# Performance work log

Hardware: AMD Instinct MI355X
Metric: run time of the kernel (lower is better)

## Reference

```python
import jax, jax.numpy as jnp
import numpy as np

B, L, D = 2, 1024, 1024
N = 64                 # ssm_state_dim
R = (D + 15) // 16     # dt_rank = ceil(dim/16) = 64
EPS = 1e-6


def setup_inputs() -> dict:
    key = jax.random.key(0)
    ks = jax.random.split(key, 12)
    s = 0.02
    return {
        "x": jax.random.normal(ks[0], (B, L, D), dtype=jnp.float32),
        "norm_w": jnp.ones((D,), jnp.float32),
        "Wx": jax.random.normal(ks[1], (R + 2 * N, D), jnp.float32) * s,
        "dtW": jax.random.normal(ks[2], (D, R), jnp.float32) * s,
        "dtb": jax.random.normal(ks[3], (D,), jnp.float32) * s,
        "A_log": jnp.zeros((D, N), jnp.float32),
        "Dskip": jnp.ones((D,), jnp.float32),
        "Wout": jax.random.normal(ks[4], (D, D), jnp.float32) * s,
        "selW": jax.random.normal(ks[5], (D, D), jnp.float32) * s,
        "selb": jax.random.normal(ks[6], (D,), jnp.float32) * s,
        "sel_gate": jnp.ones((D,), jnp.float32),
        "impW": jax.random.normal(ks[7], (N, D), jnp.float32) * s,
        "impb": jax.random.normal(ks[8], (N,), jnp.float32) * s,
        "gateW": jax.random.normal(ks[9], (D, D), jnp.float32) * s,
        "gateb": jax.random.normal(ks[10], (D,), jnp.float32) * s,
    }


def _rmsnorm(x, w):
    return x * jax.lax.rsqrt(jnp.mean(x * x, axis=-1, keepdims=True) + EPS) * w


def reference(x, norm_w, Wx, dtW, dtb, A_log, Dskip, Wout, selW, selb,
              sel_gate, impW, impb, gateW, gateb):
    xn = _rmsnorm(x, norm_w)                       # [B,L,D]
    xp = jnp.einsum('bld,kd->blk', xn, Wx)         # [B,L,R+2N]
    delta_r = xp[..., :R]
    B_ssm = xp[..., R:R + N]
    C_ssm = xp[..., R + N:]

    # selective masking
    sel = jax.nn.sigmoid((jnp.einsum('bld,kd->blk', xn, selW) + selb) * sel_gate)
    xn = xn * sel
    imp = jax.nn.sigmoid(jnp.einsum('bld,nd->bln', xn, impW) + impb)  # [B,L,N]

    delta = jax.nn.softplus(jnp.einsum('blr,dr->bld', delta_r, dtW) + dtb)  # [B,L,D]
    A = -jnp.exp(A_log)                            # [D,N]

    # gated update
    gate = jax.nn.sigmoid(jnp.einsum('bld,kd->blk', xn, gateW) + gateb)
    xn = xn * gate

    B_ssm = B_ssm * imp
    C_ssm = C_ssm * imp

    def step(h, inp):
        dt, bt, ct, xt = inp                       # [B,D],[B,N],[B,N],[B,D]
        dA = jnp.exp(dt[:, :, None] * A)           # [B,D,N]
        h = dA * h + dt[:, :, None] * bt[:, None, :] * xt[:, :, None]
        y = jnp.einsum('bdn,bn->bd', h, ct)
        return h, y

    h0 = jnp.zeros((B, D, N), x.dtype)
    xs = (jnp.moveaxis(delta, 1, 0), jnp.moveaxis(B_ssm, 1, 0),
          jnp.moveaxis(C_ssm, 1, 0), jnp.moveaxis(xn, 1, 0))
    _, ys = jax.lax.scan(step, h0, xs)             # ys: [L,B,D]
    y = jnp.moveaxis(ys, 0, 1)                     # [B,L,D]

    return jnp.einsum('bld,kd->blk', y + x * Dskip, Wout)
```

## Files before the change

### kernel.cpp

```cpp
#include <hip/hip_runtime.h>

typedef __attribute__((ext_vector_type(8))) short short8;
typedef __attribute__((ext_vector_type(4))) float f32x4;
typedef unsigned short u16;

__device__ __forceinline__ u16 f2bf(float f){
  unsigned int u = __float_as_uint(f);
  u += 0x7FFFu + ((u>>16)&1u);
  return (u16)(u>>16);
}
__device__ __forceinline__ float bf2f(u16 h){
  return __uint_as_float(((unsigned int)h)<<16);
}
__device__ __forceinline__ float sigm(float x){ return 1.f/(1.f+__expf(-x)); }

__device__ __forceinline__ float fexp2(float x){
#if __has_builtin(__builtin_amdgcn_exp2f)
  return __builtin_amdgcn_exp2f(x);
#else
  float r; asm("v_exp_f32 %0, %1" : "=v"(r) : "v"(x)); return r;
#endif
}

__device__ __forceinline__ void gl_lds(const u16* g, u16* l){
  __builtin_amdgcn_global_load_lds(
      (const __attribute__((address_space(1))) void*)g,
      (__attribute__((address_space(3))) void*)l, 16, 0, 0);
}

#define MDIM 2048
#define DDIM 1024
#define KDIM 1024
#define LOG2E 1.44269504f
#define NCHUNK 32
#define TCH 32
#define CVT_TOTAL 3473408

__global__ __launch_bounds__(256) void pre_k(
    const float* __restrict__ x, const float* __restrict__ nw,
    const float* __restrict__ selW, const float* __restrict__ Wx,
    const float* __restrict__ gateW, const float* __restrict__ impW,
    const float* __restrict__ Wout, const float* __restrict__ dtW,
    u16* __restrict__ xn,
    u16* __restrict__ dA, u16* __restrict__ dB, u16* __restrict__ dC,
    u16* __restrict__ dD)
{
  const int bx = blockIdx.x, tid = threadIdx.x;
  if (bx < 2048){
    float4 xv = ((const float4*)(x + (size_t)bx*DDIM))[tid];
    float s = xv.x*xv.x + xv.y*xv.y + xv.z*xv.z + xv.w*xv.w;
    #pragma unroll
    for (int m=1; m<64; m<<=1) s += __shfl_xor(s, m);
    __shared__ float red[4];
    if ((tid&63)==0) red[tid>>6] = s;
    __syncthreads();
    float tot = red[0]+red[1]+red[2]+red[3];
    float rs = rsqrtf(tot*(1.f/1024.f) + 1e-6f);
    float4 wv = ((const float4*)nw)[tid];
    ushort4 o;
    o.x=f2bf(xv.x*rs*wv.x); o.y=f2bf(xv.y*rs*wv.y);
    o.z=f2bf(xv.z*rs*wv.z); o.w=f2bf(xv.w*rs*wv.w);
    ((ushort4*)(xn + (size_t)bx*DDIM))[tid] = o;
  } else {
    int e = ((bx-2048)*256 + tid)*4;
    if (e >= CVT_TOTAL) return;
    const float4* s; u16* d;
    if (e < 1048576){ s=(const float4*)(selW+e); d=dA+e; }
    else if (e < 1245184){ int o=e-1048576; s=(const float4*)(Wx+o); d=dA+1048576+o; }
    else if (e < 2293760){ int o=e-1245184; s=(const float4*)(gateW+o); d=dB+o; }
    else if (e < 2359296){ int o=e-2293760; s=(const float4*)(impW+o); d=dB+1048576+o; }
    else if (e < 3407872){ int o=e-2359296; s=(const float4*)(Wout+o); d=dC+o; }
    else { int o=e-3407872; s=(const float4*)(dtW+o); d=dD+o; }
    float4 v = *s;
    ushort4 ov; ov.x=f2bf(v.x); ov.y=f2bf(v.y); ov.z=f2bf(v.z); ov.w=f2bf(v.w);
    *(ushort4*)d = ov;
  }
}

template<int MODE>
__device__ __forceinline__ void gemm_body(
    u16* smem,
    const u16* __restrict__ X, const u16* __restrict__ W,
    const float* __restrict__ b1, const float* __restrict__ b2,
    const float* __restrict__ b3, const u16* __restrict__ aux,
    u16* __restrict__ oBF, u16* __restrict__ oBF2,
    float* __restrict__ oF1, float* __restrict__ oF2, float* __restrict__ oF3)
{
  u16* const AsP[2] = { smem, smem + 4096 };
  u16* const BsP[2] = { smem + 8192, smem + 12288 };
  const int tid = threadIdx.x;
  const int wid = tid>>6, lane = tid&63;
  const int wr = wid>>1, wc = wid&1;
  const int lr = lane&15, lg = lane>>4;

  const int nx = gridDim.x;
  const int nwg = nx*gridDim.y;
  const int lin = blockIdx.y*nx + blockIdx.x;
  const int lt = (lin&7)*(nwg>>3) + (lin>>3);
  const int bm = (lt/nx)*64, bn = (lt%nx)*64;

  f32x4 acc[2][2];
  #pragma unroll
  for (int a0=0;a0<2;++a0)
    #pragma unroll
    for (int b0=0;b0<2;++b0) acc[a0][b0] = (f32x4){0.f,0.f,0.f,0.f};

  const int srow = wid*8 + (lane>>3);
  const int kslot = 8*((lane&7) ^ (lane>>3));
  const u16* ag = X + (size_t)(bm + srow)*KDIM + kslot;
  const u16* bg = W + (size_t)(bn + srow)*KDIM + kslot;
  const int lofs = wid*512;

  auto stage = [&](int buf, int kt){
    gl_lds(ag + kt, AsP[buf] + lofs);
    gl_lds(ag + (size_t)32*KDIM + kt, AsP[buf] + 2048 + lofs);
    gl_lds(bg + kt, BsP[buf] + lofs);
    gl_lds(bg + (size_t)32*KDIM + kt, BsP[buf] + 2048 + lofs);
  };

  stage(0, 0);
  stage(1, 64);
  asm volatile("s_waitcnt vmcnt(4)" ::: "memory");
  __builtin_amdgcn_s_barrier();

  int cur = 0;
  #pragma unroll
  for (int kt=0; kt<KDIM; kt+=64){
    short8 af[2][2], bfr[2][2];
    #pragma unroll
    for (int a0=0;a0<2;++a0){
      const int R = wr*32 + a0*16 + lr;
      #pragma unroll
      for (int kh=0;kh<2;++kh)
        af[a0][kh] = *(const short8*)(AsP[cur] + R*64 + ((kh*32 + lg*8) ^ ((lr&7)<<3)));
    }
    #pragma unroll
    for (int b0=0;b0<2;++b0){
      const int R = wc*32 + b0*16 + lr;
      #pragma unroll
      for (int kh=0;kh<2;++kh)
        bfr[b0][kh] = *(const short8*)(BsP[cur] + R*64 + ((kh*32 + lg*8) ^ ((lr&7)<<3)));
    }
    asm volatile("s_waitcnt lgkmcnt(0)" ::: "memory");
    __builtin_amdgcn_sched_barrier(0);
    __builtin_amdgcn_s_barrier();
    if (kt < KDIM-128)
      stage(cur, kt+128);
    #pragma unroll
    for (int kh=0;kh<2;++kh)
      #pragma unroll
      for (int a0=0;a0<2;++a0)
        #pragma unroll
        for (int b0=0;b0<2;++b0)
          acc[a0][b0] = __builtin_amdgcn_mfma_f32_16x16x32_bf16(af[a0][kh], bfr[b0][kh], acc[a0][b0], 0, 0, 0);
    __builtin_amdgcn_sched_barrier(0);
    if (kt < KDIM-128){
      asm volatile("s_waitcnt vmcnt(4)" ::: "memory");
      __builtin_amdgcn_s_barrier();
    } else if (kt < KDIM-64){
      asm volatile("s_waitcnt vmcnt(0)" ::: "memory");
      __builtin_amdgcn_s_barrier();
    }
    cur ^= 1;
  }

  const int colb = bn + wc*32;
  #pragma unroll
  for (int a0=0;a0<2;++a0){
    const int m0 = bm + wr*32 + a0*16 + lg*4;
    #pragma unroll
    for (int b0=0;b0<2;++b0){
      const int n = colb + b0*16 + lr;
      #pragma unroll
      for (int i=0;i<4;++i){
        const int m = m0 + i;
        float v = acc[a0][b0][i];
        if constexpr (MODE==0){
          if (n < 1024){
            float s = sigm((v + b1[n])*b2[n]);
            float xnv = bf2f(aux[(size_t)m*1024 + n]);
            oBF[(size_t)m*1024 + n] = f2bf(xnv*s);
          } else if (n < 1088){
            oBF2[(size_t)m*64 + (n-1024)] = f2bf(v);
          } else {
            oF2[(size_t)m*128 + (n-1088)] = v;
          }
        } else if constexpr (MODE==1){
          if (n < 1024){
            float g = sigm(v + b1[n]);
            oBF[(size_t)m*1024 + n] = f2bf(bf2f(aux[(size_t)m*1024 + n])*g);
          } else {
            int c = n-1024;
            float it = sigm(v + b2[c]);
            float bb = b3[(size_t)m*128 + c];
            float cc = b3[(size_t)m*128 + 64 + c];
            oF2[(size_t)m*64 + c] = bb*it;
            oF3[(size_t)m*64 + c] = cc*it;
          }
        } else {
          oF1[(size_t)m*1024 + n] = v;
        }
      }
    }
  }
}

template<int MODE>
__global__ __launch_bounds__(256) void gemm_bt(
    const u16* __restrict__ X, const u16* __restrict__ W,
    const float* __restrict__ b1, const float* __restrict__ b2,
    const float* __restrict__ b3, const u16* __restrict__ aux,
    u16* __restrict__ oBF, u16* __restrict__ oBF2,
    float* __restrict__ oF1, float* __restrict__ oF2, float* __restrict__ oF3)
{
  __shared__ __align__(16) u16 pool[16384];
  gemm_body<MODE>(pool, X, W, b1, b2, b3, aux, oBF, oBF2, oF1, oF2, oF3);
}

__global__ __launch_bounds__(256) void gemm1d_k(
    const u16* __restrict__ xn2, const u16* __restrict__ wsB,
    const float* __restrict__ gateb, const float* __restrict__ impb,
    const float* __restrict__ BCb,
    u16* __restrict__ xn316, float* __restrict__ BIp, float* __restrict__ CIp,
    const u16* __restrict__ dr, const u16* __restrict__ dtWb,
    const float* __restrict__ dtb, u16* __restrict__ delta16)
{
  __shared__ __align__(16) u16 pool[16384];
  if (blockIdx.z == 0){
    gemm_body<1>(pool, xn2, wsB, gateb, impb, BCb, xn2,
                 xn316, nullptr, nullptr, BIp, CIp);
    return;
  }
  if (blockIdx.x >= 16) return;
  u16* As = pool;
  u16* Bs = pool + 4096;
  const int tid = threadIdx.x;
  const int wid = tid>>6, lane = tid&63;
  const int wr = wid>>1, wc = wid&1;
  const int lr = lane&15, lg = lane>>4;
  const int bm = blockIdx.y*64, bn = blockIdx.x*64;

  const int srow = wid*8 + (lane>>3);
  const int kslot = 8*((lane&7) ^ (lane>>3));
  const u16* ag = dr   + (size_t)(bm + srow)*64 + kslot;
  const u16* bg = dtWb + (size_t)(bn + srow)*64 + kslot;
  const int lofs = wid*512;

  gl_lds(ag, As + lofs);
  gl_lds(ag + 32*64, As + 2048 + lofs);
  gl_lds(bg, Bs + lofs);
  gl_lds(bg + 32*64, Bs + 2048 + lofs);
  asm volatile("s_waitcnt vmcnt(0)" ::: "memory");
  __builtin_amdgcn_s_barrier();

  f32x4 acc[2][2];
  #pragma unroll
  for (int a0=0;a0<2;++a0)
    #pragma unroll
    for (int b0=0;b0<2;++b0) acc[a0][b0] = (f32x4){0.f,0.f,0.f,0.f};

  short8 af[2][2], bfr[2][2];
  #pragma unroll
  for (int a0=0;a0<2;++a0){
    const int R = wr*32 + a0*16 + lr;
    #pragma unroll
    for (int kh=0;kh<2;++kh)
      af[a0][kh] = *(const short8*)(As + R*64 + ((kh*32 + lg*8) ^ ((lr&7)<<3)));
  }
  #pragma unroll
  for (int b0=0;b0<2;++b0){
    const int R = wc*32 + b0*16 + lr;
    #pragma unroll
    for (int kh=0;kh<2;++kh)
      bfr[b0][kh] = *(const short8*)(Bs + R*64 + ((kh*32 + lg*8) ^ ((lr&7)<<3)));
  }
  #pragma unroll
  for (int kh=0;kh<2;++kh)
    #pragma unroll
    for (int a0=0;a0<2;++a0)
      #pragma unroll
      for (int b0=0;b0<2;++b0)
        acc[a0][b0] = __builtin_amdgcn_mfma_f32_16x16x32_bf16(af[a0][kh], bfr[b0][kh], acc[a0][b0], 0, 0, 0);

  #pragma unroll
  for (int a0=0;a0<2;++a0){
    const int m0 = bm + wr*32 + a0*16 + lg*4;
    #pragma unroll
    for (int b0=0;b0<2;++b0){
      const int n = bn + wc*32 + b0*16 + lr;
      const float bias = dtb[n];
      #pragma unroll
      for (int i=0;i<4;++i){
        float t = acc[a0][b0][i] + bias;
        float sp = fmaxf(t,0.f) + log1pf(__expf(-fabsf(t)));
        delta16[(size_t)(m0+i)*1024 + n] = f2bf(sp);
      }
    }
  }
}

__global__ __launch_bounds__(256) void scan_p1(
    const u16* __restrict__ delta, const u16* __restrict__ xn3,
    const float* __restrict__ BI, const float* __restrict__ A_log,
    u16* __restrict__ hst, float* __restrict__ sumdt)
{
  const int tid = threadIdx.x;
  const int lane = tid & 63;
  const int wv = __builtin_amdgcn_readfirstlane(tid >> 6);
  const int dg = blockIdx.x, c = blockIdx.y, b = blockIdx.z;
  const int d = dg*64 + lane;
  const int nb = wv*16;
  float A2[16], h[16];
  #pragma unroll
  for (int n0=0;n0<4;++n0){
    float4 al = *(const float4*)(A_log + (size_t)d*64 + nb + n0*4);
    A2[n0*4+0] = -__expf(al.x)*LOG2E;
    A2[n0*4+1] = -__expf(al.y)*LOG2E;
    A2[n0*4+2] = -__expf(al.z)*LOG2E;
    A2[n0*4+3] = -__expf(al.w)*LOG2E;
  }
  #pragma unroll
  for (int n=0;n<16;++n) h[n]=0.f;
  const int row0 = b*1024 + c*TCH;
  float sdt = 0.f;
  for (int t=0;t<TCH;++t){
    const size_t row = row0 + t;
    float dt = bf2f(delta[row*1024 + d]);
    float xt = bf2f(xn3[row*1024 + d]);
    sdt += dt;
    float k = dt*xt;
    const float* bi = BI + row*64 + nb;
    #pragma unroll
    for (int n=0;n<16;++n)
      h[n] = fexp2(dt*A2[n])*h[n] + k*bi[n];
  }
  if (wv==0) sumdt[(size_t)(c*2+b)*1024 + d] = sdt;
  #pragma unroll
  for (int n=0;n<16;++n)
    hst[(size_t)((c*2+b)*64 + nb + n)*1024 + d] = f2bf(h[n]);
}

__global__ __launch_bounds__(256) void scan_p2(
    const float* __restrict__ A_log, const float* __restrict__ sumdt,
    u16* __restrict__ hst)
{
  int gid = blockIdx.x*256 + threadIdx.x;
  int d = gid & 1023, n = (gid>>10)&63, b = gid>>16;
  float A2 = -__expf(A_log[(size_t)d*64 + n])*LOG2E;
  float carry = 0.f;
  #pragma unroll
  for (int c=0;c<NCHUNK;++c){
    float P = fexp2(A2 * sumdt[(size_t)(c*2+b)*1024 + d]);
    size_t off = (size_t)((c*2+b)*64 + n)*1024 + d;
    float he = bf2f(hst[off]);
    hst[off] = f2bf(carry);
    carry = P*carry + he;
  }
}

__global__ __launch_bounds__(256) void scan_p3(
    const u16* __restrict__ delta, const u16* __restrict__ xn3,
    const float* __restrict__ BI, const float* __restrict__ CI,
    const float* __restrict__ A_log, const float* __restrict__ x,
    const float* __restrict__ Dskip, const u16* __restrict__ hst,
    u16* __restrict__ z)
{
  __shared__ float ypart[4][TCH][64];
  const int tid = threadIdx.x;
  const int lane = tid & 63;
  const int wv = __builtin_amdgcn_readfirstlane(tid >> 6);
  const int dg = blockIdx.x, c = blockIdx.y, b = blockIdx.z;
  const int d = dg*64 + lane;
  const int nb = wv*16;
  float A2[16], h[16];
  #pragma unroll
  for (int n0=0;n0<4;++n0){
    float4 al = *(const float4*)(A_log + (size_t)d*64 + nb + n0*4);
    A2[n0*4+0] = -__expf(al.x)*LOG2E;
    A2[n0*4+1] = -__expf(al.y)*LOG2E;
    A2[n0*4+2] = -__expf(al.z)*LOG2E;
    A2[n0*4+3] = -__expf(al.w)*LOG2E;
  }
  #pragma unroll
  for (int n=0;n<16;++n)
    h[n] = bf2f(hst[(size_t)((c*2+b)*64 + nb + n)*1024 + d]);
  const int row0 = b*1024 + c*TCH;
  for (int t=0;t<TCH;++t){
    const size_t row = row0 + t;
    float dt = bf2f(delta[row*1024 + d]);
    float xt = bf2f(xn3[row*1024 + d]);
    float k = dt*xt;
    const float* bi = BI + row*64 + nb;
    const float* ci = CI + row*64 + nb;
    float y0=0.f, y1=0.f, y2=0.f, y3=0.f;
    #pragma unroll
    for (int n=0;n<16;n+=4){
      h[n+0] = fexp2(dt*A2[n+0])*h[n+0] + k*bi[n+0];  y0 += h[n+0]*ci[n+0];
      h[n+1] = fexp2(dt*A2[n+1])*h[n+1] + k*bi[n+1];  y1 += h[n+1]*ci[n+1];
      h[n+2] = fexp2(dt*A2[n+2])*h[n+2] + k*bi[n+2];  y2 += h[n+2]*ci[n+2];
      h[n+3] = fexp2(dt*A2[n+3])*h[n+3] + k*bi[n+3];  y3 += h[n+3]*ci[n+3];
    }
    ypart[wv][t][lane] = (y0+y1)+(y2+y3);
  }
  __syncthreads();
  const int dbase = dg*64;
  #pragma unroll
  for (int i=0;i<8;++i){
    int idx = tid + i*256;
    int t = idx>>6, dl = idx&63;
    size_t row = row0 + t;
    float y = ypart[0][t][dl] + ypart[1][t][dl] + ypart[2][t][dl] + ypart[3][t][dl];
    float xr = x[row*1024 + dbase + dl];
    z[row*1024 + dbase + dl] = f2bf(y + xr*Dskip[dbase+dl]);
  }
}

extern "C" void kernel_launch(void* const* d_in, const int* in_sizes, int n_in,
                              void* d_out, int out_size, void* d_ws, size_t ws_size,
                              hipStream_t stream) {
  const float* x       = (const float*)d_in[0];
  const float* norm_w  = (const float*)d_in[1];
  const float* Wx      = (const float*)d_in[2];
  const float* dtW     = (const float*)d_in[3];
  const float* dtb     = (const float*)d_in[4];
  const float* A_log   = (const float*)d_in[5];
  const float* Dskip   = (const float*)d_in[6];
  const float* Wout    = (const float*)d_in[7];
  const float* selW    = (const float*)d_in[8];
  const float* selb    = (const float*)d_in[9];
  const float* sel_gate= (const float*)d_in[10];
  const float* impW    = (const float*)d_in[11];
  const float* impb    = (const float*)d_in[12];
  const float* gateW   = (const float*)d_in[13];
  const float* gateb   = (const float*)d_in[14];
  float* out = (float*)d_out;

  char* w = (char*)d_ws;
  u16*  wsA   = (u16*)(w);
  u16*  wsB   = (u16*)(w + 2490368);
  u16*  wsC   = (u16*)(w + 4718592);
  u16*  wsD   = (u16*)(w + 6815744);
  u16*  xn    = (u16*)(w + 6946816);
  u16*  xn2   = (u16*)(w + 11141120);
  u16*  hst   = (u16*)(w + 6946816);
  u16*  dr    = (u16*)(w + 15335424);
  u16*  delta16=(u16*)(w + 15597568);
  u16*  xn316 = (u16*)(w + 19791872);
  float* BCb  = (float*)(w + 23986176);
  float* sdt  = (float*)(w + 23986176);
  float* BIp  = (float*)(w + 25034752);
  float* CIp  = (float*)(w + 25559040);
  u16*  zb    = (u16*)(w + 26083328);

  pre_k<<<2048+3392, 256, 0, stream>>>(x, norm_w, selW, Wx, gateW, impW, Wout, dtW,
                                       xn, wsA, wsB, wsC, wsD);
  gemm_bt<0><<<dim3(19,32), 256, 0, stream>>>(xn, wsA, selb, sel_gate, nullptr, xn,
                                              xn2, dr, nullptr, BCb, nullptr);
  gemm1d_k<<<dim3(17,32,2), 256, 0, stream>>>(xn2, wsB, gateb, impb, BCb,
                                              xn316, BIp, CIp,
                                              dr, wsD, dtb, delta16);
  scan_p1<<<dim3(16,NCHUNK,2), 256, 0, stream>>>(delta16, xn316, BIp, A_log, hst, sdt);
  scan_p2<<<512, 256, 0, stream>>>(A_log, sdt, hst);
  scan_p3<<<dim3(16,NCHUNK,2), 256, 0, stream>>>(delta16, xn316, BIp, CIp, A_log, x, Dskip, hst, zb);
  gemm_bt<2><<<dim3(16,32), 256, 0, stream>>>(zb, wsC, nullptr, nullptr, nullptr, nullptr,
                                              nullptr, nullptr, out, nullptr, nullptr);
}
```

Measured before the change: 111.4 us.

## Give each GEMM wave private LDS tiles and drop workgroup barriers; unroll scan loops

```diff
diff --git a/kernel.cpp b/kernel.cpp
--- a/kernel.cpp
+++ b/kernel.cpp
@@ -86,8 +86,6 @@
     u16* __restrict__ oBF, u16* __restrict__ oBF2,
     float* __restrict__ oF1, float* __restrict__ oF2, float* __restrict__ oF3)
 {
-  u16* const AsP[2] = { smem, smem + 4096 };
-  u16* const BsP[2] = { smem + 8192, smem + 12288 };
   const int tid = threadIdx.x;
   const int wid = tid>>6, lane = tid&63;
   const int wr = wid>>1, wc = wid&1;
@@ -105,63 +103,51 @@
     #pragma unroll
     for (int b0=0;b0<2;++b0) acc[a0][b0] = (f32x4){0.f,0.f,0.f,0.f};
 
-  const int srow = wid*8 + (lane>>3);
-  const int kslot = 8*((lane&7) ^ (lane>>3));
-  const u16* ag = X + (size_t)(bm + srow)*KDIM + kslot;
-  const u16* bg = W + (size_t)(bn + srow)*KDIM + kslot;
-  const int lofs = wid*512;
+  u16* const wbase = smem + wid*4096;
+
+  const int srow = lane>>2;
+  const int scol = 8*((lane&3) ^ ((lane>>3)&3));
+  const u16* ag = X + (size_t)(bm + wr*32 + srow)*KDIM + scol;
+  const u16* bg = W + (size_t)(bn + wc*32 + srow)*KDIM + scol;
 
   auto stage = [&](int buf, int kt){
-    gl_lds(ag + kt, AsP[buf] + lofs);
-    gl_lds(ag + (size_t)32*KDIM + kt, AsP[buf] + 2048 + lofs);
-    gl_lds(bg + kt, BsP[buf] + lofs);
-    gl_lds(bg + (size_t)32*KDIM + kt, BsP[buf] + 2048 + lofs);
+    gl_lds(ag + kt,                   wbase + buf*1024);
+    gl_lds(ag + (size_t)16*KDIM + kt, wbase + buf*1024 + 512);
+    gl_lds(bg + kt,                   wbase + 2048 + buf*1024);
+    gl_lds(bg + (size_t)16*KDIM + kt, wbase + 2048 + buf*1024 + 512);
   };
 
+  const int rsw = (lg ^ ((lr>>1)&3))*8;
+  const int off0 = lr*32 + rsw;
+  const int off1 = (16+lr)*32 + rsw;
+
   stage(0, 0);
-  stage(1, 64);
+  stage(1, 32);
   asm volatile("s_waitcnt vmcnt(4)" ::: "memory");
-  __builtin_amdgcn_s_barrier();
-
-  int cur = 0;
-  #pragma unroll
-  for (int kt=0; kt<KDIM; kt+=64){
-    short8 af[2][2], bfr[2][2];
-    #pragma unroll
-    for (int a0=0;a0<2;++a0){
-      const int R = wr*32 + a0*16 + lr;
-      #pragma unroll
-      for (int kh=0;kh<2;++kh)
-        af[a0][kh] = *(const short8*)(AsP[cur] + R*64 + ((kh*32 + lg*8) ^ ((lr&7)<<3)));
-    }
-    #pragma unroll
-    for (int b0=0;b0<2;++b0){
-      const int R = wc*32 + b0*16 + lr;
-      #pragma unroll
-      for (int kh=0;kh<2;++kh)
-        bfr[b0][kh] = *(const short8*)(BsP[cur] + R*64 + ((kh*32 + lg*8) ^ ((lr&7)<<3)));
-    }
+
+  #pragma unroll
+  for (int t=0; t<32; ++t){
+    const int cur = t&1;
+    const u16* Ab = wbase + cur*1024;
+    const u16* Bb = wbase + 2048 + cur*1024;
+    short8 a0f = *(const short8*)(Ab + off0);
+    short8 a1f = *(const short8*)(Ab + off1);
+    short8 b0f = *(const short8*)(Bb + off0);
+    short8 b1f = *(const short8*)(Bb + off1);
     asm volatile("s_waitcnt lgkmcnt(0)" ::: "memory");
     __builtin_amdgcn_sched_barrier(0);
-    __builtin_amdgcn_s_barrier();
-    if (kt < KDIM-128)
-      stage(cur, kt+128);
-    #pragma unroll
-    for (int kh=0;kh<2;++kh)
-      #pragma unroll
-      for (int a0=0;a0<2;++a0)
-        #pragma unroll
-        for (int b0=0;b0<2;++b0)
-          acc[a0][b0] = __builtin_amdgcn_mfma_f32_16x16x32_bf16(af[a0][kh], bfr[b0][kh], acc[a0][b0], 0, 0, 0);
+    if (t < 30)
+      stage(cur, (t+2)*32);
+    acc[0][0] = __builtin_amdgcn_mfma_f32_16x16x32_bf16(a0f, b0f, acc[0][0], 0, 0, 0);
+    acc[0][1] = __builtin_amdgcn_mfma_f32_16x16x32_bf16(a0f, b1f, acc[0][1], 0, 0, 0);
+    acc[1][0] = __builtin_amdgcn_mfma_f32_16x16x32_bf16(a1f, b0f, acc[1][0], 0, 0, 0);
+    acc[1][1] = __builtin_amdgcn_mfma_f32_16x16x32_bf16(a1f, b1f, acc[1][1], 0, 0, 0);
     __builtin_amdgcn_sched_barrier(0);
-    if (kt < KDIM-128){
+    if (t < 30){
       asm volatile("s_waitcnt vmcnt(4)" ::: "memory");
-      __builtin_amdgcn_s_barrier();
-    } else if (kt < KDIM-64){
+    } else if (t == 30){
       asm volatile("s_waitcnt vmcnt(0)" ::: "memory");
-      __builtin_amdgcn_s_barrier();
     }
-    cur ^= 1;
   }
 
   const int colb = bn + wc*32;
@@ -323,6 +309,7 @@
   for (int n=0;n<16;++n) h[n]=0.f;
   const int row0 = b*1024 + c*TCH;
   float sdt = 0.f;
+  #pragma unroll 2
   for (int t=0;t<TCH;++t){
     const size_t row = row0 + t;
     float dt = bf2f(delta[row*1024 + d]);
@@ -385,6 +372,7 @@
   for (int n=0;n<16;++n)
     h[n] = bf2f(hst[(size_t)((c*2+b)*64 + nb + n)*1024 + d]);
   const int row0 = b*1024 + c*TCH;
+  #pragma unroll 2
   for (int t=0;t<TCH;++t){
     const size_t row = row0 + t;
     float dt = bf2f(delta[row*1024 + d]);
```

After: 125.5 us. 12.7% more time.
